# Optimization experiments

Measured on AMD Instinct MI355X. Metric: run time of the kernel, lower is better.

## Reference

```python
import jax, jax.numpy as jnp
import numpy as np

M, C = 100000, 24
LINE_W, LENGTH_W, REPROJ_W = 0.0, 0.0, 1.0  # forward() default weights


def setup_inputs() -> dict:
    ks = jax.random.split(jax.random.key(0), 8)
    # 3 pole markers per frame, centered ~5m in front of cameras (positive depth)
    pole3d = 0.5 * jax.random.normal(ks[0], (M, 3, 3), jnp.float32) + jnp.array([0.0, 0.0, 5.0], jnp.float32)
    # intrinsics: fx=fy~1000, principal point ~(960,540)
    fx = 1000.0 + 10.0 * jax.random.normal(ks[1], (C,), jnp.float32)
    fy = 1000.0 + 10.0 * jax.random.normal(ks[2], (C,), jnp.float32)
    u0 = 960.0 + 5.0 * jax.random.normal(ks[3], (C,), jnp.float32)
    v0 = 540.0 + 5.0 * jax.random.normal(ks[4], (C,), jnp.float32)
    K = jnp.zeros((C, 3, 3), jnp.float32)
    K = K.at[:, 0, 0].set(fx).at[:, 1, 1].set(fy).at[:, 0, 2].set(u0).at[:, 1, 2].set(v0).at[:, 2, 2].set(1.0)
    dist = 0.01 * jax.random.normal(ks[5], (C, 5), jnp.float32)  # k1,k2,p1,p2,k3
    R = jnp.eye(3, dtype=jnp.float32)[None] + 0.01 * jax.random.normal(ks[6], (C, 3, 3), jnp.float32)
    t = 0.1 * jax.random.normal(ks[7], (C, 3), jnp.float32)
    # detected pixels in a 1920x1080 frame
    pole2d = jax.random.uniform(jax.random.fold_in(ks[0], 1), (M, C, 3, 2), jnp.float32) * jnp.array([1920.0, 1080.0], jnp.float32)
    # visibility mask; guarantee >=1 visible camera per frame (matches non-empty loss_reproj)
    mask = jax.random.randint(jax.random.fold_in(ks[0], 2), (M, C), 0, 2, jnp.int32).at[:, 0].set(1)
    pole = jnp.array([0.5, 0.5], jnp.float32)  # [d1, d2] in meters
    return {"pole3d": pole3d, "pole2d": pole2d, "K": K, "dist": dist, "R": R, "t": t, "pole": pole, "mask": mask}


def _project(X, K, R, t, dist):
    # X: [M,P,3] world points; outputs pixels [M,C,P,2]
    xc = jnp.einsum('cij,mpj->mcpi', R, X) + t[None, :, None, :]   # camera frame
    xn = xc[..., :2] / xc[..., 2:3]                                # perspective divide
    x0, x1 = xn[..., 0], xn[..., 1]
    r2 = x0 * x0 + x1 * x1
    k1, k2, p1, p2, k3 = (dist[:, i][None, :, None] for i in range(5))
    radial = 1.0 + k1 * r2 + k2 * r2 * r2 + k3 * r2 * r2 * r2
    xu = x0 * radial + 2.0 * p1 * x0 * x1 + p2 * (r2 + 2.0 * x0 * x0)
    yu = x1 * radial + p1 * (r2 + 2.0 * x1 * x1) + 2.0 * p2 * x0 * x1
    fx = K[:, 0, 0][None, :, None]; fy = K[:, 1, 1][None, :, None]
    u0 = K[:, 0, 2][None, :, None]; v0 = K[:, 1, 2][None, :, None]
    return jnp.stack([fx * xu + u0, fy * yu + v0], axis=-1)


def reference(pole3d, pole2d, K, dist, R, t, pole, mask):
    d1, d2 = pole[0], pole[1]
    dsum = d1 + d2
    # wand geometry loss per frame
    expect_mid = (d2 * pole3d[:, 0] + d1 * pole3d[:, 2]) / dsum            # [M,3]
    loss_line = jnp.linalg.norm(pole3d[:, 1] - expect_mid, axis=-1)        # [M]
    loss_length = jnp.abs(jnp.linalg.norm(pole3d[:, 0] - pole3d[:, 2], axis=-1) - dsum)
    loss_wand = LINE_W * loss_line + LENGTH_W * loss_length                # [M]
    # reprojection loss
    proj = _project(pole3d, K, R, t, dist)                                 # [M,C,3,2]
    per_cam = REPROJ_W * jnp.linalg.norm(pole2d - proj, axis=-1).mean(axis=-1)  # [M,C]
    m = mask.astype(per_cam.dtype)
    loss_reproj = (per_cam * m).sum(axis=-1) / m.sum(axis=-1)              # masked mean over cams
    return jnp.mean(loss_wand + loss_reproj)
```

## Files before the change

kernel.cpp:

```cpp
#include <hip/hip_runtime.h>

#define MM 100000
#define CC 24
#define BLK 256
#define WPB (BLK / 64)
#define GRID 1024
#define NW (GRID * WPB)
#define NP (MM / 2)

#define P2S (2 * NW * CC * 6)
#define P3S (2 * NW * 9)
#define MSS (2 * NW * CC)

struct Pack {
    float2 a0, a1, a2;
    float  w;
    float  q[9];
};

__device__ __forceinline__ Pack load_pack(
    const float* __restrict__ p2p, const float* __restrict__ p3p,
    const int* __restrict__ msp, float active)
{
    Pack pk;
    const float2* pd = (const float2*)p2p;
    pk.a0 = pd[0]; pk.a1 = pd[1]; pk.a2 = pd[2];
    pk.w  = active * (float)(*msp);
    #pragma unroll
    for (int i = 0; i < 9; ++i) pk.q[i] = p3p[i];
    return pk;
}

__device__ __forceinline__ void pin(const Pack& p) {
    asm volatile("" ::
        "v"(p.a0.x), "v"(p.a0.y), "v"(p.a1.x), "v"(p.a1.y),
        "v"(p.a2.x), "v"(p.a2.y), "v"(p.w),
        "v"(p.q[0]), "v"(p.q[1]), "v"(p.q[2]), "v"(p.q[3]), "v"(p.q[4]),
        "v"(p.q[5]), "v"(p.q[6]), "v"(p.q[7]), "v"(p.q[8]));
}

__global__ __launch_bounds__(BLK) void ba_main_kernel(
    const float* __restrict__ pole3d,
    const float* __restrict__ pole2d,
    const float* __restrict__ Kmat,
    const float* __restrict__ dist,
    const float* __restrict__ Rmat,
    const float* __restrict__ tvec,
    const int*   __restrict__ mask,
    float* __restrict__ ws)
{
    const int tid  = threadIdx.x;
    const int lane = tid & 63;
    const int half = lane >> 5;
    const int cl   = lane & 31;
    const int c    = (cl < CC) ? cl : (CC - 1);
    const float active = (cl < CC) ? 1.f : 0.f;

    const float fx = Kmat[c * 9 + 0], fy = Kmat[c * 9 + 4];
    const float u0 = Kmat[c * 9 + 2], v0 = Kmat[c * 9 + 5];
    const float k1 = dist[c * 5 + 0], k2 = dist[c * 5 + 1];
    const float p1 = dist[c * 5 + 2], p2 = dist[c * 5 + 3], k3 = dist[c * 5 + 4];
    const float r00 = Rmat[c * 9 + 0], r01 = Rmat[c * 9 + 1], r02 = Rmat[c * 9 + 2];
    const float r10 = Rmat[c * 9 + 3], r11 = Rmat[c * 9 + 4], r12 = Rmat[c * 9 + 5];
    const float r20 = Rmat[c * 9 + 6], r21 = Rmat[c * 9 + 7], r22 = Rmat[c * 9 + 8];
    const float t0 = tvec[c * 3 + 0], t1 = tvec[c * 3 + 1], t2 = tvec[c * 3 + 2];

    const int wid = blockIdx.x * WPB + (tid >> 6);

    const int m0 = 2 * wid + half;
    const float* p2p = pole2d + ((size_t)m0 * CC + c) * 6;
    const float* p3p = pole3d + (size_t)m0 * 9;
    const int*   msp = mask + (size_t)m0 * CC + c;

    float acc = 0.f;

    auto consume = [&](const Pack& pk) {
        float s = 0.f;
        #pragma unroll
        for (int i = 0; i < 3; ++i) {
            const float X = pk.q[3 * i + 0], Y = pk.q[3 * i + 1], Z = pk.q[3 * i + 2];
            const float xc = r00 * X + r01 * Y + r02 * Z + t0;
            const float yc = r10 * X + r11 * Y + r12 * Z + t1;
            const float zc = r20 * X + r21 * Y + r22 * Z + t2;
            const float inv = __builtin_amdgcn_rcpf(zc);
            const float x0 = xc * inv, x1 = yc * inv;
            const float r2 = x0 * x0 + x1 * x1;
            const float radial = 1.f + r2 * (k1 + r2 * (k2 + r2 * k3));
            const float xu = x0 * radial + 2.f * p1 * x0 * x1 + p2 * (r2 + 2.f * x0 * x0);
            const float yu = x1 * radial + p1 * (r2 + 2.f * x1 * x1) + 2.f * p2 * x0 * x1;
            const float uu = fx * xu + u0;
            const float vv = fy * yu + v0;
            const float dx = (i == 0 ? pk.a0.x : i == 1 ? pk.a1.x : pk.a2.x) - uu;
            const float dy = (i == 0 ? pk.a0.y : i == 1 ? pk.a1.y : pk.a2.y) - vv;
            s += __builtin_amdgcn_sqrtf(dx * dx + dy * dy);
        }
        const unsigned long long ball = __ballot(pk.w != 0.f);
        const unsigned wcnt = half ? __popcll(ball >> 32)
                                   : __popcll(ball & 0xFFFFFFFFull);
        acc += s * pk.w * __builtin_amdgcn_rcpf((float)(3u * wcnt));
    };

    Pack cur = load_pack(p2p, p3p, msp, active);
    pin(cur);

    for (int p = wid; p + NW < NP; p += NW) {
        Pack nxt = load_pack(p2p + P2S, p3p + P3S, msp + MSS, active);
        pin(nxt);
        consume(cur);
        p2p += P2S; p3p += P3S; msp += MSS;
        cur = nxt;
    }
    consume(cur);

    float tot = acc;
    #pragma unroll
    for (int d = 1; d < 64; d <<= 1) tot += __shfl_xor(tot, d);

    __shared__ float sh[WPB];
    if (lane == 0) sh[tid >> 6] = tot;
    __syncthreads();
    if (tid == 0) {
        float bl = 0.f;
        #pragma unroll
        for (int j = 0; j < WPB; ++j) bl += sh[j];
        ws[blockIdx.x] = bl;
    }
}

__global__ __launch_bounds__(256) void ba_reduce_kernel(
    const float* __restrict__ ws, float* __restrict__ out)
{
    __shared__ float sh[256];
    float s = 0.f;
    for (int i = threadIdx.x; i < GRID; i += 256) s += ws[i];
    sh[threadIdx.x] = s;
    __syncthreads();
    #pragma unroll
    for (int st = 128; st > 0; st >>= 1) {
        if (threadIdx.x < st) sh[threadIdx.x] += sh[threadIdx.x + st];
        __syncthreads();
    }
    if (threadIdx.x == 0) out[0] = sh[0] * (1.0f / MM);
}

extern "C" void kernel_launch(void* const* d_in, const int* in_sizes, int n_in,
                              void* d_out, int out_size, void* d_ws, size_t ws_size,
                              hipStream_t stream) {
    const float* pole3d = (const float*)d_in[0];
    const float* pole2d = (const float*)d_in[1];
    const float* Kmat   = (const float*)d_in[2];
    const float* dist   = (const float*)d_in[3];
    const float* Rmat   = (const float*)d_in[4];
    const float* tvec   = (const float*)d_in[5];
    const int*   mask   = (const int*)d_in[7];
    float* out = (float*)d_out;
    float* ws  = (float*)d_ws;

    ba_main_kernel<<<GRID, BLK, 0, stream>>>(
        pole3d, pole2d, Kmat, dist, Rmat, tvec, mask, ws);
    ba_reduce_kernel<<<1, 256, 0, stream>>>(ws, out);
}
```

Before: 26.42 us.

## Process two frames per half-wave per iteration with packed float2 math

Each half-wave now handles two consecutive frames per loop step instead of one. Their loads are batched into one prefetched pack, which doubles the memory requests in flight per thread. The projection arithmetic is written on 2-wide float vectors so the compiler can emit packed FP32 FMAs for the two frames, and the 2*p1/2*p2 constants are hoisted. The trade-off is higher register pressure from the larger prefetch buffer, which may lower occupancy. It also needs two ballots per step.

```diff
diff --git a/kernel.cpp b/kernel.cpp
--- a/kernel.cpp
+++ b/kernel.cpp
@@ -6,16 +6,19 @@
 #define WPB (BLK / 64)
 #define GRID 1024
 #define NW (GRID * WPB)
-#define NP (MM / 2)
+#define NQ (MM / 4)
 
-#define P2S (2 * NW * CC * 6)
-#define P3S (2 * NW * 9)
-#define MSS (2 * NW * CC)
+#define P2S (4 * NW * CC * 6)
+#define P3S (4 * NW * 9)
+#define MSS (4 * NW * CC)
+
+typedef float f2 __attribute__((ext_vector_type(2)));
 
 struct Pack {
-    float2 a0, a1, a2;
-    float  w;
-    float  q[9];
+    f2 a0[3];
+    f2 a1[3];
+    f2 w01;
+    f2 q01[9];
 };
 
 __device__ __forceinline__ Pack load_pack(
@@ -23,20 +26,33 @@
     const int* __restrict__ msp, float active)
 {
     Pack pk;
-    const float2* pd = (const float2*)p2p;
-    pk.a0 = pd[0]; pk.a1 = pd[1]; pk.a2 = pd[2];
-    pk.w  = active * (float)(*msp);
+    const f2* pd0 = (const f2*)p2p;
+    const f2* pd1 = (const f2*)(p2p + CC * 6);
     #pragma unroll
-    for (int i = 0; i < 9; ++i) pk.q[i] = p3p[i];
+    for (int i = 0; i < 3; ++i) { pk.a0[i] = pd0[i]; pk.a1[i] = pd1[i]; }
+    pk.w01.x = active * (float)msp[0];
+    pk.w01.y = active * (float)msp[CC];
+    #pragma unroll
+    for (int i = 0; i < 9; ++i) {
+        pk.q01[i].x = p3p[i];
+        pk.q01[i].y = p3p[9 + i];
+    }
     return pk;
 }
 
 __device__ __forceinline__ void pin(const Pack& p) {
     asm volatile("" ::
-        "v"(p.a0.x), "v"(p.a0.y), "v"(p.a1.x), "v"(p.a1.y),
-        "v"(p.a2.x), "v"(p.a2.y), "v"(p.w),
-        "v"(p.q[0]), "v"(p.q[1]), "v"(p.q[2]), "v"(p.q[3]), "v"(p.q[4]),
-        "v"(p.q[5]), "v"(p.q[6]), "v"(p.q[7]), "v"(p.q[8]));
+        "v"(p.a0[0].x), "v"(p.a0[0].y), "v"(p.a0[1].x), "v"(p.a0[1].y),
+        "v"(p.a0[2].x), "v"(p.a0[2].y),
+        "v"(p.a1[0].x), "v"(p.a1[0].y), "v"(p.a1[1].x), "v"(p.a1[1].y),
+        "v"(p.a1[2].x), "v"(p.a1[2].y),
+        "v"(p.w01.x), "v"(p.w01.y));
+    asm volatile("" ::
+        "v"(p.q01[0].x), "v"(p.q01[0].y), "v"(p.q01[1].x), "v"(p.q01[1].y),
+        "v"(p.q01[2].x), "v"(p.q01[2].y), "v"(p.q01[3].x), "v"(p.q01[3].y),
+        "v"(p.q01[4].x), "v"(p.q01[4].y), "v"(p.q01[5].x), "v"(p.q01[5].y),
+        "v"(p.q01[6].x), "v"(p.q01[6].y), "v"(p.q01[7].x), "v"(p.q01[7].y),
+        "v"(p.q01[8].x), "v"(p.q01[8].y));
 }
 
 __global__ __launch_bounds__(BLK) void ba_main_kernel(
@@ -58,8 +74,9 @@
 
     const float fx = Kmat[c * 9 + 0], fy = Kmat[c * 9 + 4];
     const float u0 = Kmat[c * 9 + 2], v0 = Kmat[c * 9 + 5];
-    const float k1 = dist[c * 5 + 0], k2 = dist[c * 5 + 1];
-    const float p1 = dist[c * 5 + 2], p2 = dist[c * 5 + 3], k3 = dist[c * 5 + 4];
+    const float k1 = dist[c * 5 + 0], k2 = dist[c * 5 + 1], k3 = dist[c * 5 + 4];
+    const float p1 = dist[c * 5 + 2], p2 = dist[c * 5 + 3];
+    const float tp1 = 2.f * p1, tp2 = 2.f * p2;
     const float r00 = Rmat[c * 9 + 0], r01 = Rmat[c * 9 + 1], r02 = Rmat[c * 9 + 2];
     const float r10 = Rmat[c * 9 + 3], r11 = Rmat[c * 9 + 4], r12 = Rmat[c * 9 + 5];
     const float r20 = Rmat[c * 9 + 6], r21 = Rmat[c * 9 + 7], r22 = Rmat[c * 9 + 8];
@@ -67,7 +84,7 @@
 
     const int wid = blockIdx.x * WPB + (tid >> 6);
 
-    const int m0 = 2 * wid + half;
+    const int m0 = 4 * wid + 2 * half;
     const float* p2p = pole2d + ((size_t)m0 * CC + c) * 6;
     const float* p3p = pole3d + (size_t)m0 * 9;
     const int*   msp = mask + (size_t)m0 * CC + c;
@@ -75,35 +92,43 @@
     float acc = 0.f;
 
     auto consume = [&](const Pack& pk) {
-        float s = 0.f;
+        float sA = 0.f, sB = 0.f;
         #pragma unroll
         for (int i = 0; i < 3; ++i) {
-            const float X = pk.q[3 * i + 0], Y = pk.q[3 * i + 1], Z = pk.q[3 * i + 2];
-            const float xc = r00 * X + r01 * Y + r02 * Z + t0;
-            const float yc = r10 * X + r11 * Y + r12 * Z + t1;
-            const float zc = r20 * X + r21 * Y + r22 * Z + t2;
-            const float inv = __builtin_amdgcn_rcpf(zc);
-            const float x0 = xc * inv, x1 = yc * inv;
-            const float r2 = x0 * x0 + x1 * x1;
-            const float radial = 1.f + r2 * (k1 + r2 * (k2 + r2 * k3));
-            const float xu = x0 * radial + 2.f * p1 * x0 * x1 + p2 * (r2 + 2.f * x0 * x0);
-            const float yu = x1 * radial + p1 * (r2 + 2.f * x1 * x1) + 2.f * p2 * x0 * x1;
-            const float uu = fx * xu + u0;
-            const float vv = fy * yu + v0;
-            const float dx = (i == 0 ? pk.a0.x : i == 1 ? pk.a1.x : pk.a2.x) - uu;
-            const float dy = (i == 0 ? pk.a0.y : i == 1 ? pk.a1.y : pk.a2.y) - vv;
-            s += __builtin_amdgcn_sqrtf(dx * dx + dy * dy);
+            const f2 X = pk.q01[3 * i + 0], Y = pk.q01[3 * i + 1], Z = pk.q01[3 * i + 2];
+            const f2 xc = r00 * X + r01 * Y + r02 * Z + t0;
+            const f2 yc = r10 * X + r11 * Y + r12 * Z + t1;
+            const f2 zc = r20 * X + r21 * Y + r22 * Z + t2;
+            f2 inv;
+            inv.x = __builtin_amdgcn_rcpf(zc.x);
+            inv.y = __builtin_amdgcn_rcpf(zc.y);
+            const f2 x0 = xc * inv, x1 = yc * inv;
+            const f2 r2 = x0 * x0 + x1 * x1;
+            const f2 radial = 1.f + r2 * (k1 + r2 * (k2 + r2 * k3));
+            const f2 x0x1 = x0 * x1;
+            const f2 tx = r2 + 2.f * x0 * x0;
+            const f2 ty = r2 + 2.f * x1 * x1;
+            const f2 xu = x0 * radial + tp1 * x0x1 + p2 * tx;
+            const f2 yu = x1 * radial + tp2 * x0x1 + p1 * ty;
+            const f2 uu = fx * xu + u0;
+            const f2 vv = fy * yu + v0;
+            const float dxA = pk.a0[i].x - uu.x, dyA = pk.a0[i].y - vv.x;
+            sA += __builtin_amdgcn_sqrtf(dxA * dxA + dyA * dyA);
+            const float dxB = pk.a1[i].x - uu.y, dyB = pk.a1[i].y - vv.y;
+            sB += __builtin_amdgcn_sqrtf(dxB * dxB + dyB * dyB);
         }
-        const unsigned long long ball = __ballot(pk.w != 0.f);
-        const unsigned wcnt = half ? __popcll(ball >> 32)
-                                   : __popcll(ball & 0xFFFFFFFFull);
-        acc += s * pk.w * __builtin_amdgcn_rcpf((float)(3u * wcnt));
+        const unsigned long long bx = __ballot(pk.w01.x != 0.f);
+        const unsigned long long by = __ballot(pk.w01.y != 0.f);
+        const unsigned wA = half ? __popcll(bx >> 32) : __popcll(bx & 0xFFFFFFFFull);
+        const unsigned wB = half ? __popcll(by >> 32) : __popcll(by & 0xFFFFFFFFull);
+        acc += sA * pk.w01.x * __builtin_amdgcn_rcpf((float)(3u * wA))
+             + sB * pk.w01.y * __builtin_amdgcn_rcpf((float)(3u * wB));
     };
 
     Pack cur = load_pack(p2p, p3p, msp, active);
     pin(cur);
 
-    for (int p = wid; p + NW < NP; p += NW) {
+    for (int p = wid; p + NW < NQ; p += NW) {
         Pack nxt = load_pack(p2p + P2S, p3p + P3S, msp + MSS, active);
         pin(nxt);
         consume(cur);
```

Measured after the change: 23.61 us. -10.6%, faster.
